# Kernel optimization log

Measured on AMD Instinct MI355X. Metric: run time of the kernel, lower is better.

Reference implementation:

```python
import jax, jax.numpy as jnp
import numpy as np

B, C, H, W = 16, 256, 56, 56
WH, WW = 7, 7
NH = 8            # heads
HID = 1024        # mlp hidden = int(4*dim)
N = WH * WW
EPS = 1e-5


def _rel_index():
    # mirrors the torch buffer computation in Rel_Attention.__init__
    coords = np.stack(np.meshgrid(np.arange(WH), np.arange(WW), indexing='ij')).reshape(2, -1)  # (2, N)
    rel = coords[:, :, None] - coords[:, None, :]  # (2, N, N)
    rel[0] += WH - 1
    rel[1] += WW - 1
    rel[0] *= 2 * WW - 1
    return jnp.asarray(rel.sum(0).reshape(-1))  # (N*N,)

REL_IDX = _rel_index()


def channel_ln(x, w, b):
    # LayerNorm over channel dim of NCHW tensor (permute -> LN -> permute back)
    xt = x.transpose(0, 2, 3, 1)  # BHWC
    mu = xt.mean(-1, keepdims=True)
    var = xt.var(-1, keepdims=True)
    xt = (xt - mu) / jnp.sqrt(var + EPS) * w + b
    return xt.transpose(0, 3, 1, 2)


def to_blocks(x):
    # (B,C,H,W) -> (B, H/wh, W/ww, C, wh, ww)
    b, c, h, w = x.shape
    x = x.reshape(b, c, h // WH, WH, w // WW, WW)
    return x.transpose(0, 2, 4, 1, 3, 5)


def unblock(x):
    # faithful to original: reshape(B, C, Hb*win_W, Hb*win_W)  (square sizes)
    b, hb, wb, c, wh, ww = x.shape
    return x.transpose(0, 3, 1, 4, 2, 5).reshape(b, c, hb * ww, hb * ww)


def rel_attention(xw, qkv_w, qkv_b, proj_w, proj_b, table):
    b, hb, wb, c = xw.shape[:4]
    hd = c // NH
    scale = hd ** (-0.5)
    xf = xw.reshape(-1, c, N)                                  # (M, C, N)
    qkv = jnp.einsum('oc,mcn->mon', qkv_w, xf) + qkv_b[None, :, None]
    q, k, v = jnp.split(qkv, 3, axis=1)

    def heads(t):
        return t.reshape(-1, NH, hd, N).transpose(0, 1, 3, 2)  # (M, h, N, d)

    q, k, v = heads(q), heads(k), heads(v)
    bias = table[REL_IDX].reshape(N, N, NH).transpose(2, 0, 1)  # (h, N, N)
    attn = jnp.einsum('mhnd,mhkd->mhnk', q, k) * scale + bias
    attn = jax.nn.softmax(attn, axis=-1)
    o = jnp.einsum('mhnk,mhkd->mhnd', attn, v)                 # (M, h, N, d)
    o = o.transpose(0, 1, 3, 2).reshape(-1, c, N)              # (M, C, N)
    o = jnp.einsum('oc,mcn->mon', proj_w, o) + proj_b[None, :, None]
    return o.reshape(b, hb, wb, c, WH, WW)


def mlp(x, fc1_w, fc1_b, fc2_w, fc2_b):
    h = jnp.einsum('oc,bchw->bohw', fc1_w, x) + fc1_b[None, :, None, None]
    h = jax.nn.gelu(h, approximate=False)
    return jnp.einsum('oc,bchw->bohw', fc2_w, h) + fc2_b[None, :, None, None]


def setup_inputs() -> dict:
    key = jax.random.key(0)
    ks = jax.random.split(key, 8)
    s = 0.02
    return {
        'x': jax.random.normal(ks[0], (B, C, H, W), jnp.float32),
        'ln1_w': jnp.ones((C,), jnp.float32),
        'ln1_b': jnp.zeros((C,), jnp.float32),
        'ln2_w': jnp.ones((C,), jnp.float32),
        'ln2_b': jnp.zeros((C,), jnp.float32),
        'qkv_w': jax.random.normal(ks[1], (3 * C, C), jnp.float32) * s,
        'qkv_b': jnp.zeros((3 * C,), jnp.float32),
        'proj_w': jax.random.normal(ks[2], (C, C), jnp.float32) * s,
        'proj_b': jnp.zeros((C,), jnp.float32),
        'rel_bias_table': jax.random.normal(ks[3], ((2 * WH - 1) * (2 * WW - 1), NH), jnp.float32) * s,
        'fc1_w': jax.random.normal(ks[4], (HID, C), jnp.float32) * s,
        'fc1_b': jnp.zeros((HID,), jnp.float32),
        'fc2_w': jax.random.normal(ks[5], (C, HID), jnp.float32) * s,
        'fc2_b': jnp.zeros((C,), jnp.float32),
    }


def reference(x, ln1_w, ln1_b, ln2_w, ln2_b, qkv_w, qkv_b, proj_w, proj_b,
              rel_bias_table, fc1_w, fc1_b, fc2_w, fc2_b):
    out = to_blocks(channel_ln(x, ln1_w, ln1_b))
    out = rel_attention(out, qkv_w, qkv_b, proj_w, proj_b, rel_bias_table)
    # original applies attn a second time before unblocking
    out = rel_attention(out, qkv_w, qkv_b, proj_w, proj_b, rel_bias_table)
    x = x + unblock(out)
    x = x + mlp(channel_ln(x, ln2_w, ln2_b), fc1_w, fc1_b, fc2_w, fc2_b)
    return x
```

## Files before the change

### kernel.cpp

```cpp
#include <hip/hip_runtime.h>
#include <stdint.h>

typedef uint16_t u16;
typedef short bf16x4 __attribute__((ext_vector_type(4)));
typedef short bf16x8 __attribute__((ext_vector_type(8)));
typedef float f32x4 __attribute__((ext_vector_type(4)));

__device__ __forceinline__ float bf2f(u16 s) {
  union { unsigned int i; float f; } c; c.i = ((unsigned int)s) << 16; return c.f;
}
__device__ __forceinline__ u16 f2bf(float f) {
  union { float f; unsigned int i; } c; c.f = f;
  unsigned int u = c.i;
  u += 0x7FFFu + ((u >> 16) & 1u);
  return (u16)(u >> 16);
}
__device__ __forceinline__ f32x4 mfma16(bf16x8 a, bf16x8 b, f32x4 c) {
  return __builtin_amdgcn_mfma_f32_16x16x32_bf16(a, b, c, 0, 0, 0);
}
__device__ __forceinline__ int dtype_flag(const u16* ln1w_raw) { return ln1w_raw[0] == 0x3F80 ? 1 : 0; }
__device__ __forceinline__ float loadF(const void* p, size_t i, int flag) {
  return flag ? bf2f(((const u16*)p)[i]) : ((const float*)p)[i];
}

#define OFF_QKVW 0
#define OFF_QKVB 196608
#define OFF_PROJW 197376
#define OFF_PROJB 262912
#define OFF_REL 263168
#define OFF_FC1W 264520
#define OFF_FC1B 526664
#define OFF_FC2W 527688
#define OFF_FC2B 789832
#define OFF_LN1W 790088
#define OFF_LN1B 790344
#define OFF_LN2W 790600
#define OFF_LN2B 790856
#define WC_TOTAL 791112

__global__ __launch_bounds__(256) void k_convert(const u16* __restrict__ ln1w_raw,
    const void* qkvw, const void* qkvb, const void* projw, const void* projb,
    const void* rel, const void* fc1w, const void* fc1b, const void* fc2w, const void* fc2b,
    const void* ln1w, const void* ln1b, const void* ln2w, const void* ln2b,
    u16* __restrict__ dst) {
  const int flag = dtype_flag(ln1w_raw);
  int i = blockIdx.x * 256 + threadIdx.x;
  if (i >= WC_TOTAL) return;
  const void* src; int off;
  if      (i < OFF_QKVB)  { src = qkvw;  off = i - OFF_QKVW; }
  else if (i < OFF_PROJW) { src = qkvb;  off = i - OFF_QKVB; }
  else if (i < OFF_PROJB) { src = projw; off = i - OFF_PROJW; }
  else if (i < OFF_REL)   { src = projb; off = i - OFF_PROJB; }
  else if (i < OFF_FC1W)  { src = rel;   off = i - OFF_REL; }
  else if (i < OFF_FC1B)  { src = fc1w;  off = i - OFF_FC1W; }
  else if (i < OFF_FC2W)  { src = fc1b;  off = i - OFF_FC1B; }
  else if (i < OFF_FC2B)  { src = fc2w;  off = i - OFF_FC2W; }
  else if (i < OFF_LN1W)  { src = fc2b;  off = i - OFF_FC2B; }
  else if (i < OFF_LN1B)  { src = ln1w;  off = i - OFF_LN1W; }
  else if (i < OFF_LN2W)  { src = ln1b;  off = i - OFF_LN1B; }
  else if (i < OFF_LN2B)  { src = ln2w;  off = i - OFF_LN2W; }
  else                    { src = ln2b;  off = i - OFF_LN2B; }
  if (i < OFF_QKVB) {
    int j = off & 7, li = (off >> 3) & 63, c0i = (off >> 9) & 7, grp = off >> 12;
    off = (grp * 16 + (li & 15)) * 256 + c0i * 32 + (li >> 4) * 8 + j;
  } else if (i >= OFF_PROJW && i < OFF_PROJB) {
    int j = off & 7, li = (off >> 3) & 63, c0i = (off >> 9) & 7, grp = off >> 12;
    off = (grp * 16 + (li & 15)) * 256 + c0i * 32 + (li >> 4) * 8 + j;
  } else if (i >= OFF_FC1W && i < OFF_FC1B) {
    int j = off & 7, li = (off >> 3) & 63, hj = (off >> 9) & 1, c0i = (off >> 10) & 7,
        w = (off >> 13) & 3, ch = off >> 15;
    off = (ch * 128 + w * 32 + hj * 16 + (li & 15)) * 256 + c0i * 32 + (li >> 4) * 8 + j;
  } else if (i >= OFF_FC2W && i < OFF_FC2B) {
    int j = off & 7, li = (off >> 3) & 63, oct = (off >> 9) & 3, kki = (off >> 11) & 3,
        ch = (off >> 13) & 7, w = off >> 16;
    off = (w * 64 + oct * 16 + (li & 15)) * 1024 + ch * 128 + kki * 32 + (li >> 4) * 8 + j;
  }
  dst[i] = flag ? ((const u16*)src)[off] : f2bf(((const float*)src)[off]);
}

__global__ __launch_bounds__(256) void k_ln1b(const void* __restrict__ xin,
                                              const u16* __restrict__ ln1w_raw,
                                              const u16* __restrict__ lw,
                                              const u16* __restrict__ lb,
                                              u16* __restrict__ win) {
  const int flag = dtype_flag(ln1w_raw);
  __shared__ float tile[56 * 257];
  __shared__ float smu[56], srs[56];
  const int bid = blockIdx.x;
  const int b = bid / 56, h = bid - b * 56;
  const int t = threadIdx.x;
  const int hb = h / 7, ph = h - hb * 7;
  if (!flag) {
#pragma unroll
    for (int i = 0; i < 14; ++i) {
      int chunk = i * 256 + t;
      int c = chunk / 14, w4 = (chunk - c * 14) * 4;
      const float* xp4 = (const float*)xin + ((size_t)(b * 256 + c) * 56 + h) * 56 + w4;
      f32x4 v = *(const f32x4*)xp4;
#pragma unroll
      for (int k = 0; k < 4; ++k) tile[(w4 + k) * 257 + c] = v[k];
    }
  } else {
#pragma unroll
    for (int i = 0; i < 7; ++i) {
      int chunk = i * 256 + t;
      int c = chunk / 7, w8 = (chunk - c * 7) * 8;
      const u16* xp8 = (const u16*)xin + ((size_t)(b * 256 + c) * 56 + h) * 56 + w8;
      bf16x8 v = *(const bf16x8*)xp8;
#pragma unroll
      for (int k = 0; k < 8; ++k) tile[(w8 + k) * 257 + c] = bf2f((u16)v[k]);
    }
  }
  __syncthreads();
  {
    const int row = t >> 2, qq = t & 3;
    float s = 0.f, q = 0.f;
    if (row < 56) {
      const float* tr = &tile[row * 257 + qq];
#pragma unroll 8
      for (int c0 = 0; c0 < 64; ++c0) { float v = tr[c0 * 4]; s += v; q += v * v; }
    }
    s += __shfl_xor(s, 1, 64); q += __shfl_xor(q, 1, 64);
    s += __shfl_xor(s, 2, 64); q += __shfl_xor(q, 2, 64);
    if (row < 56 && qq == 0) {
      float mm = s * (1.f / 256.f);
      float var = q * (1.f / 256.f) - mm * mm;
      smu[row] = mm; srs[row] = rsqrtf(var + 1e-5f);
    }
  }
  __syncthreads();
#pragma unroll
  for (int i = 0; i < 7; ++i) {
    int eid8 = i * 256 + t;
    int wp = eid8 >> 5, c8 = (eid8 & 31) << 3;
    const float mm = smu[wp], rs = srs[wp];
    const int m = b * 64 + hb * 8 + (wp / 7), n = ph * 7 + (wp % 7);
    bf16x8 o;
#pragma unroll
    for (int j = 0; j < 8; ++j) {
      int c = c8 + j;
      o[j] = (short)f2bf((tile[wp * 257 + c] - mm) * rs * bf2f(lw[c]) + bf2f(lb[c]));
    }
    *(bf16x8*)&win[(size_t)m * 12544 + n * 256 + c8] = o;
  }
}

__global__ __launch_bounds__(512) void k_attn_stage(const u16* __restrict__ win,
                                                    const u16* __restrict__ qkvw,
                                                    const u16* __restrict__ qkvb,
                                                    const u16* __restrict__ rel,
                                                    const u16* __restrict__ projw,
                                                    const u16* __restrict__ projb,
                                                    u16* __restrict__ wout) {
  __shared__ __align__(16) u16 xs[64 * 264];
  __shared__ __align__(16) u16 wa[8][7424];
  const int m = blockIdx.x;
  const int t = threadIdx.x;
  const int w = t >> 6, li = t & 63, lane = li & 15, quad = li >> 4;
  const int hg = w;
  const f32x4 z = {0.f, 0.f, 0.f, 0.f};
  const u16* src = win + (size_t)m * 12544;
#pragma unroll
  for (int i = 0; i < 4; ++i) {
    int chunk = i * 512 + t;
    if (chunk < 1568) {
      int n = chunk >> 5, cc = (chunk & 31) << 3;
      *(bf16x8*)&xs[n * 264 + cc] = *(const bf16x8*)&src[chunk << 3];
    }
  }
  for (int i = t; i < 15 * 264; i += 512) xs[49 * 264 + i] = 0;
  u16* qw = wa[w];
  u16* kw = wa[w] + 2560;
  u16* vw = wa[w] + 5120;
  u16* Pw = wa[w];
  u16* Os = xs;
  for (int i = li; i < 15 * 40; i += 64) { qw[49 * 40 + i] = 0; kw[49 * 40 + i] = 0; }
  for (int i = li; i < 32 * 15; i += 64) { int d = i / 15, j = i - d * 15; vw[d * 72 + 49 + j] = 0; }
  __syncthreads();
  const float SCALE = 0.17677669529663687f;
#pragma unroll
  for (int part = 0; part < 2; ++part) {
    const int obase = part * 256 + hg * 32;
    f32x4 acc[4][2];
#pragma unroll
    for (int i = 0; i < 4; ++i) { acc[i][0] = z; acc[i][1] = z; }
#pragma unroll
    for (int c0i = 0; c0i < 8; ++c0i) {
      bf16x8 a[4], b[2];
#pragma unroll
      for (int nt = 0; nt < 4; ++nt)
        a[nt] = *(const bf16x8*)&xs[(nt * 16 + lane) * 264 + c0i * 32 + quad * 8];
#pragma unroll
      for (int oj = 0; oj < 2; ++oj)
        b[oj] = *(const bf16x8*)&qkvw[(size_t)(((part * 16 + hg * 2 + oj) * 8 + c0i) * 64 + li) * 8];
      __builtin_amdgcn_s_setprio(1);
#pragma unroll
      for (int nt = 0; nt < 4; ++nt)
#pragma unroll
        for (int oj = 0; oj < 2; ++oj) acc[nt][oj] = mfma16(a[nt], b[oj], acc[nt][oj]);
      __builtin_amdgcn_s_setprio(0);
    }
    u16* dstL = part ? kw : qw;
#pragma unroll
    for (int oj = 0; oj < 2; ++oj) {
      const int d = oj * 16 + lane;
      const float bias = bf2f(qkvb[obase + d]);
#pragma unroll
      for (int nt = 0; nt < 4; ++nt)
#pragma unroll
        for (int r = 0; r < 4; ++r) {
          int n = nt * 16 + quad * 4 + r;
          if (n < 49) dstL[n * 40 + d] = f2bf(acc[nt][oj][r] + bias);
        }
    }
  }
  {
    f32x4 acc[2][4];
#pragma unroll
    for (int i = 0; i < 2; ++i)
#pragma unroll
      for (int j = 0; j < 4; ++j) acc[i][j] = z;
#pragma unroll
    for (int c0i = 0; c0i < 8; ++c0i) {
      bf16x8 a[2], b[4];
#pragma unroll
      for (int vj = 0; vj < 2; ++vj)
        a[vj] = *(const bf16x8*)&qkvw[(size_t)(((32 + hg * 2 + vj) * 8 + c0i) * 64 + li) * 8];
#pragma unroll
      for (int nt = 0; nt < 4; ++nt)
        b[nt] = *(const bf16x8*)&xs[(nt * 16 + lane) * 264 + c0i * 32 + quad * 8];
      __builtin_amdgcn_s_setprio(1);
#pragma unroll
      for (int vj = 0; vj < 2; ++vj)
#pragma unroll
        for (int nt = 0; nt < 4; ++nt) acc[vj][nt] = mfma16(a[vj], b[nt], acc[vj][nt]);
      __builtin_amdgcn_s_setprio(0);
    }
#pragma unroll
    for (int vj = 0; vj < 2; ++vj)
#pragma unroll
      for (int r = 0; r < 4; ++r) {
        const int d = vj * 16 + quad * 4 + r;
        const float bias = bf2f(qkvb[512 + hg * 32 + d]);
#pragma unroll
        for (int nt = 0; nt < 4; ++nt) {
          int n = nt * 16 + lane;
          if (n < 49) vw[d * 72 + n] = f2bf(acc[vj][nt][r] + bias);
        }
      }
  }
  __syncthreads();
  f32x4 s[4][4];
  {
    bf16x8 aq[4], bk[4];
#pragma unroll
    for (int nt = 0; nt < 4; ++nt) {
      aq[nt] = *(const bf16x8*)&qw[(nt * 16 + lane) * 40 + quad * 8];
      bk[nt] = *(const bf16x8*)&kw[(nt * 16 + lane) * 40 + quad * 8];
    }
    __builtin_amdgcn_s_setprio(1);
#pragma unroll
    for (int i = 0; i < 4; ++i)
#pragma unroll
      for (int j = 0; j < 4; ++j) s[i][j] = mfma16(aq[i], bk[j], z);
    __builtin_amdgcn_s_setprio(0);
  }
#pragma unroll
  for (int nt1 = 0; nt1 < 4; ++nt1) {
#pragma unroll
    for (int r = 0; r < 4; ++r) {
      int n1 = nt1 * 16 + quad * 4 + r;
      int n1c = n1 < 49 ? n1 : 48;
      int ph1 = n1c / 7, pw1 = n1c - ph1 * 7;
#pragma unroll
      for (int j = 0; j < 4; ++j) {
        int n2 = j * 16 + lane;
        float e;
        if (n2 < 49) {
          int ph2 = n2 / 7, pw2 = n2 - ph2 * 7;
          int idx = (ph1 - ph2 + 6) * 13 + (pw1 - pw2 + 6);
          e = __expf(s[nt1][j][r] * SCALE + bf2f(rel[idx * 8 + hg]));
        } else e = 0.f;
        Pw[n1 * 72 + j * 16 + lane] = f2bf(e);
      }
    }
  }
  {
    f32x4 o[4][2], ssum[4];
#pragma unroll
    for (int i = 0; i < 4; ++i) { o[i][0] = z; o[i][1] = z; ssum[i] = z; }
    bf16x8 bones;
#pragma unroll
    for (int k = 0; k < 8; ++k) bones[k] = (short)0x3F80;
#pragma unroll
    for (int kc = 0; kc < 2; ++kc) {
      bf16x8 ap[4], bv[2];
#pragma unroll
      for (int nt1 = 0; nt1 < 4; ++nt1)
        ap[nt1] = *(const bf16x8*)&Pw[(nt1 * 16 + lane) * 72 + kc * 32 + quad * 8];
#pragma unroll
      for (int dt = 0; dt < 2; ++dt)
        bv[dt] = *(const bf16x8*)&vw[(dt * 16 + lane) * 72 + kc * 32 + quad * 8];
      __builtin_amdgcn_s_setprio(1);
#pragma unroll
      for (int nt1 = 0; nt1 < 4; ++nt1) {
        ssum[nt1] = mfma16(ap[nt1], bones, ssum[nt1]);
#pragma unroll
        for (int dt = 0; dt < 2; ++dt) o[nt1][dt] = mfma16(ap[nt1], bv[dt], o[nt1][dt]);
      }
      __builtin_amdgcn_s_setprio(0);
    }
#pragma unroll
    for (int nt1 = 0; nt1 < 4; ++nt1) {
      f32x4 rv;
#pragma unroll
      for (int r = 0; r < 4; ++r) rv[r] = __builtin_amdgcn_rcpf(ssum[nt1][r]);
#pragma unroll
      for (int dt = 0; dt < 2; ++dt)
#pragma unroll
        for (int r = 0; r < 4; ++r) {
          int n1 = nt1 * 16 + quad * 4 + r;
          if (n1 < 49) Os[n1 * 264 + hg * 32 + dt * 16 + lane] = f2bf(o[nt1][dt][r] * rv[r]);
        }
    }
  }
  __syncthreads();
  {
    f32x4 acc[4][2];
#pragma unroll
    for (int i = 0; i < 4; ++i) { acc[i][0] = z; acc[i][1] = z; }
#pragma unroll
    for (int c0i = 0; c0i < 8; ++c0i) {
      bf16x8 a[4], b[2];
#pragma unroll
      for (int nt = 0; nt < 4; ++nt)
        a[nt] = *(const bf16x8*)&Os[(nt * 16 + lane) * 264 + c0i * 32 + quad * 8];
#pragma unroll
      for (int oj = 0; oj < 2; ++oj)
        b[oj] = *(const bf16x8*)&projw[(size_t)(((w * 2 + oj) * 8 + c0i) * 64 + li) * 8];
      __builtin_amdgcn_s_setprio(1);
#pragma unroll
      for (int nt = 0; nt < 4; ++nt)
#pragma unroll
        for (int oj = 0; oj < 2; ++oj) acc[nt][oj] = mfma16(a[nt], b[oj], acc[nt][oj]);
      __builtin_amdgcn_s_setprio(0);
    }
#pragma unroll
    for (int oj = 0; oj < 2; ++oj) {
      const int oc = w * 32 + oj * 16 + lane;
      const float bias = bf2f(projb[oc]);
#pragma unroll
      for (int nt = 0; nt < 4; ++nt)
#pragma unroll
        for (int r = 0; r < 4; ++r) {
          int n = nt * 16 + quad * 4 + r;
          if (n < 49) wout[(size_t)m * 12544 + n * 256 + oc] = f2bf(acc[nt][oj][r] + bias);
        }
    }
  }
}

__global__ __launch_bounds__(256) void k_resid2(const void* __restrict__ xin,
                                                const u16* __restrict__ ln1w_raw,
                                                const u16* __restrict__ attn,
                                                const u16* __restrict__ l2w,
                                                const u16* __restrict__ l2b,
                                                u16* __restrict__ xrn,
                                                u16* __restrict__ ln2d) {
  const int flag = dtype_flag(ln1w_raw);
  __shared__ float tile[56 * 257];
  __shared__ float smu[56], srs[56];
  const int bid = blockIdx.x;
  const int b = bid / 56, h = bid - b * 56;
  const int t = threadIdx.x;
  const int hb = h / 7, ph = h - hb * 7;
#pragma unroll
  for (int i = 0; i < 7; ++i) {
    int eid8 = i * 256 + t;
    int wp = eid8 >> 5, c8 = (eid8 & 31) << 3;
    int mm = b * 64 + hb * 8 + (wp / 7), nn = ph * 7 + (wp % 7);
    bf16x8 v = *(const bf16x8*)&attn[(size_t)mm * 12544 + nn * 256 + c8];
    float* dst = &tile[wp * 257 + c8];
#pragma unroll
    for (int j = 0; j < 8; ++j) dst[j] = bf2f((u16)v[j]);
  }
  __syncthreads();
  if (!flag) {
#pragma unroll
    for (int i = 0; i < 14; ++i) {
      int chunk = i * 256 + t;
      int c = chunk / 14, w4 = (chunk - c * 14) * 4;
      const size_t base = ((size_t)(b * 256 + c) * 56 + h) * 56 + w4;
      f32x4 xv = *(const f32x4*)((const float*)xin + base);
      bf16x4 o4;
#pragma unroll
      for (int k = 0; k < 4; ++k) {
        float v = tile[(w4 + k) * 257 + c] + xv[k];
        tile[(w4 + k) * 257 + c] = v;
        o4[k] = (short)f2bf(v);
      }
      *(bf16x4*)&xrn[base] = o4;
    }
  } else {
#pragma unroll
    for (int i = 0; i < 7; ++i) {
      int chunk = i * 256 + t;
      int c = chunk / 7, w8 = (chunk - c * 7) * 8;
      const size_t base = ((size_t)(b * 256 + c) * 56 + h) * 56 + w8;
      bf16x8 xv = *(const bf16x8*)((const u16*)xin + base);
      bf16x8 o8;
#pragma unroll
      for (int k = 0; k < 8; ++k) {
        float v = tile[(w8 + k) * 257 + c] + bf2f((u16)xv[k]);
        tile[(w8 + k) * 257 + c] = v;
        o8[k] = (short)f2bf(v);
      }
      *(bf16x8*)&xrn[base] = o8;
    }
  }
  __syncthreads();
  {
    const int row = t >> 2, qq = t & 3;
    float s = 0.f, q = 0.f;
    if (row < 56) {
      const float* tr = &tile[row * 257 + qq];
#pragma unroll 8
      for (int c0 = 0; c0 < 64; ++c0) { float v = tr[c0 * 4]; s += v; q += v * v; }
    }
    s += __shfl_xor(s, 1, 64); q += __shfl_xor(q, 1, 64);
    s += __shfl_xor(s, 2, 64); q += __shfl_xor(q, 2, 64);
    if (row < 56 && qq == 0) {
      float mm = s * (1.f / 256.f);
      float var = q * (1.f / 256.f) - mm * mm;
      smu[row] = mm; srs[row] = rsqrtf(var + 1e-5f);
    }
  }
  __syncthreads();
#pragma unroll
  for (int i = 0; i < 7; ++i) {
    int eid8 = i * 256 + t;
    int wp = eid8 >> 5, c8 = (eid8 & 31) << 3;
    const float mm = smu[wp], rs = srs[wp];
    bf16x8 o;
#pragma unroll
    for (int j = 0; j < 8; ++j) {
      int c = c8 + j;
      o[j] = (short)f2bf((tile[wp * 257 + c] - mm) * rs * bf2f(l2w[c]) + bf2f(l2b[c]));
    }
    const int p = b * 3136 + h * 56 + wp;
    const int pblk = p >> 6, pt = (p & 63) >> 4, r16 = p & 15;
    const int c0i = c8 >> 5, quad = (c8 >> 3) & 3;
    *(bf16x8*)&ln2d[(size_t)((((pblk * 4 + pt) * 8 + c0i) * 64 + quad * 16 + r16)) << 3] = o;
  }
}

__global__ __launch_bounds__(256, 3) void k_mlp2(const u16* __restrict__ aG,
                                                 const u16* __restrict__ w1,
                                                 const u16* __restrict__ b1,
                                                 const u16* __restrict__ w2,
                                                 const u16* __restrict__ b2,
                                                 const u16* __restrict__ xrn,
                                                 const u16* __restrict__ ln1w_raw,
                                                 void* __restrict__ out) {
  const int flag = dtype_flag(ln1w_raw);
  __shared__ __align__(16) u16 arena[25088];
  u16* xp = arena;
  u16* g  = arena + 16384;
  const int pblk = blockIdx.x;
  const int pix0 = pblk * 64;
  const int t = threadIdx.x;
  const int w = t >> 6, li = t & 63, lane = li & 15, quad = li >> 4;
  {
    const u16* asrc = aG + (size_t)pblk * 16384;
#pragma unroll
    for (int i = 0; i < 8; ++i) {
      int idx = i * 256 + t;
      *(bf16x8*)&xp[idx * 8] = *(const bf16x8*)&asrc[(size_t)idx * 8];
    }
  }
  __syncthreads();
  const f32x4 z = {0.f, 0.f, 0.f, 0.f};
  f32x4 acc2[4][4];
#pragma unroll
  for (int i = 0; i < 4; ++i)
#pragma unroll
    for (int j = 0; j < 4; ++j) acc2[i][j] = z;

  auto fc1 = [&](int ch) {
    f32x4 a1[4][2];
#pragma unroll
    for (int i = 0; i < 4; ++i) { a1[i][0] = z; a1[i][1] = z; }
#pragma unroll
    for (int c0i = 0; c0i < 8; ++c0i) {
      bf16x8 av[4], bw[2];
#pragma unroll
      for (int pt = 0; pt < 4; ++pt)
        av[pt] = *(const bf16x8*)&xp[((pt * 8 + c0i) * 64 + li) * 8];
#pragma unroll
      for (int hj = 0; hj < 2; ++hj)
        bw[hj] = *(const bf16x8*)&w1[(size_t)((((ch * 4 + w) * 8 + c0i) * 2 + hj) * 64 + li) * 8];
#pragma unroll
      for (int pt = 0; pt < 4; ++pt)
#pragma unroll
        for (int hj = 0; hj < 2; ++hj) a1[pt][hj] = mfma16(av[pt], bw[hj], a1[pt][hj]);
    }
#pragma unroll
    for (int hj = 0; hj < 2; ++hj) {
      const int hl = w * 32 + hj * 16 + lane;
      const float bias = bf2f(b1[ch * 128 + hl]);
#pragma unroll
      for (int pt = 0; pt < 4; ++pt)
#pragma unroll
        for (int r = 0; r < 4; ++r) {
          float u_ = a1[pt][hj][r] + bias;
          float y = u_ * fmaf(u_ * u_, 0.035677408136300125f, 0.7978845608028654f);
          float e2 = __expf(-2.f * y);
          float v = u_ * __builtin_amdgcn_rcpf(1.f + e2);
          g[(pt * 16 + quad * 4 + r) * 136 + hl] = f2bf(v);
        }
    }
  };
  auto fc2 = [&](int ch) {
#pragma unroll
    for (int kki = 0; kki < 4; ++kki) {
      bf16x8 aw[4], bg[4];
#pragma unroll
      for (int oct = 0; oct < 4; ++oct)
        aw[oct] = *(const bf16x8*)&w2[(size_t)((((w * 8 + ch) * 4 + kki) * 4 + oct) * 64 + li) * 8];
#pragma unroll
      for (int pt = 0; pt < 4; ++pt)
        bg[pt] = *(const bf16x8*)&g[(pt * 16 + lane) * 136 + kki * 32 + quad * 8];
#pragma unroll
      for (int oct = 0; oct < 4; ++oct)
#pragma unroll
        for (int pt = 0; pt < 4; ++pt) acc2[oct][pt] = mfma16(aw[oct], bg[pt], acc2[oct][pt]);
    }
  };

  fc1(0);
  __syncthreads();
#pragma unroll 1
  for (int ch = 0; ch < 8; ++ch) {
    fc2(ch);
    if (ch < 7) {
      __syncthreads();
      fc1(ch + 1);
      __syncthreads();
    }
  }

  float* Ob = (float*)arena;
  const int b_ = pix0 / 3136, rem0 = pix0 - b_ * 3136;
  const int sub = t & 7, r0 = t >> 3;
#pragma unroll 1
  for (int e = 0; e < 2; ++e) {
    __syncthreads();
    if ((w >> 1) == e) {
      const int wl = w & 1;
#pragma unroll
      for (int oct = 0; oct < 4; ++oct)
#pragma unroll
        for (int pt = 0; pt < 4; ++pt)
#pragma unroll
          for (int r = 0; r < 4; ++r)
            Ob[(wl * 64 + oct * 16 + quad * 4 + r) * 65 + pt * 16 + lane] = acc2[oct][pt][r];
    }
    __syncthreads();
    bf16x8 xr[4];
    size_t addrs[4];
#pragma unroll
    for (int i = 0; i < 4; ++i) {
      const int oc = e * 128 + i * 32 + r0;
      addrs[i] = (size_t)(b_ * 256 + oc) * 3136 + rem0 + sub * 8;
      xr[i] = *(const bf16x8*)&xrn[addrs[i]];
    }
#pragma unroll
    for (int i = 0; i < 4; ++i) {
      const int oc = e * 128 + i * 32 + r0;
      const float bias = bf2f(b2[oc]);
      const float* obr = &Ob[(i * 32 + r0) * 65 + sub * 8];
      float v[8];
#pragma unroll
      for (int j = 0; j < 8; ++j)
        v[j] = obr[j] + bias + bf2f((u16)xr[i][j]);
      if (flag) {
        bf16x8 o8;
#pragma unroll
        for (int j = 0; j < 8; ++j) o8[j] = (short)f2bf(v[j]);
        *(bf16x8*)&((u16*)out)[addrs[i]] = o8;
      } else {
        float* dst = &((float*)out)[addrs[i]];
        f32x4 lo = {v[0], v[1], v[2], v[3]}, hi = {v[4], v[5], v[6], v[7]};
        *(f32x4*)&dst[0] = lo;
        *(f32x4*)&dst[4] = hi;
      }
    }
  }
}

extern "C" void kernel_launch(void* const* d_in, const int* in_sizes, int n_in,
                              void* d_out, int out_size, void* d_ws, size_t ws_size,
                              hipStream_t stream) {
  (void)in_sizes; (void)n_in; (void)out_size; (void)ws_size;
  const void* x     = d_in[0];
  const u16* ln1w_raw = (const u16*)d_in[1];
  u16* ws = (u16*)d_ws;
  const size_t R = 12845056;
  u16* R0 = ws;
  u16* R1 = ws + R;
  u16* R2 = ws + 2 * R;
  u16* WC = ws + 3 * R;
  const u16* qkvw_c = WC + OFF_QKVW;
  const u16* qkvb_c = WC + OFF_QKVB;
  const u16* projw_c = WC + OFF_PROJW;
  const u16* projb_c = WC + OFF_PROJB;
  const u16* rel_c  = WC + OFF_REL;
  const u16* fc1w_c = WC + OFF_FC1W;
  const u16* fc1b_c = WC + OFF_FC1B;
  const u16* fc2w_c = WC + OFF_FC2W;
  const u16* fc2b_c = WC + OFF_FC2B;
  const u16* ln1w_c = WC + OFF_LN1W;
  const u16* ln1b_c = WC + OFF_LN1B;
  const u16* ln2w_c = WC + OFF_LN2W;
  const u16* ln2b_c = WC + OFF_LN2B;

  k_convert<<<(WC_TOTAL + 255) / 256, 256, 0, stream>>>(
      ln1w_raw, d_in[5], d_in[6], d_in[7], d_in[8], d_in[9],
      d_in[10], d_in[11], d_in[12], d_in[13], d_in[1], d_in[2], d_in[3], d_in[4], WC);

  k_ln1b      <<<896, 256, 0, stream>>>(x, ln1w_raw, ln1w_c, ln1b_c, R0);
  k_attn_stage<<<1024, 512, 0, stream>>>(R0, qkvw_c, qkvb_c, rel_c, projw_c, projb_c, R1);
  k_attn_stage<<<1024, 512, 0, stream>>>(R1, qkvw_c, qkvb_c, rel_c, projw_c, projb_c, R2);
  k_resid2    <<<896, 256, 0, stream>>>(x, ln1w_raw, R2, ln2w_c, ln2b_c, R0, R1);
  k_mlp2      <<<784, 256, 0, stream>>>(R1, fc1w_c, fc1b_c, fc2w_c, fc2b_c, R0, ln1w_raw, d_out);
}
```

Baseline: 424.0 us.

## Split attention stage into per-head-half core and separate projection kernels with fragment layout

The fused 512-thread attention kernel is split into a 256-thread attention core (two blocks per window, four heads each) and a separate projection kernel. Intermediate window activations are stored in an MFMA-fragment-ordered layout so the core can read its A/B fragments directly from global memory, without staging them in LDS or synchronising the whole block. The goal is lower LDS use and higher occupancy for the attention part. The cost is extra kernel launches, a global round-trip for the attention output, and each window's input being read twice, once per block.

```diff
diff --git a/kernel.cpp b/kernel.cpp
--- a/kernel.cpp
+++ b/kernel.cpp
@@ -21,6 +21,11 @@
 __device__ __forceinline__ int dtype_flag(const u16* ln1w_raw) { return ln1w_raw[0] == 0x3F80 ? 1 : 0; }
 __device__ __forceinline__ float loadF(const void* p, size_t i, int flag) {
   return flag ? bf2f(((const u16*)p)[i]) : ((const float*)p)[i];
+}
+
+__device__ __forceinline__ int frag_idx8(int n, int c0, int qc) {
+  return (n < 48) ? (((n >> 4) * 8 + c0) * 64 + (n & 15) + 16 * qc)
+                  : (1536 + c0 * 4 + qc);
 }
 
 #define OFF_QKVW 0
@@ -141,43 +146,34 @@
       int c = c8 + j;
       o[j] = (short)f2bf((tile[wp * 257 + c] - mm) * rs * bf2f(lw[c]) + bf2f(lb[c]));
     }
-    *(bf16x8*)&win[(size_t)m * 12544 + n * 256 + c8] = o;
-  }
-}
-
-__global__ __launch_bounds__(512) void k_attn_stage(const u16* __restrict__ win,
-                                                    const u16* __restrict__ qkvw,
-                                                    const u16* __restrict__ qkvb,
-                                                    const u16* __restrict__ rel,
-                                                    const u16* __restrict__ projw,
-                                                    const u16* __restrict__ projb,
-                                                    u16* __restrict__ wout) {
-  __shared__ __align__(16) u16 xs[64 * 264];
-  __shared__ __align__(16) u16 wa[8][7424];
-  const int m = blockIdx.x;
+    const int idx8 = frag_idx8(n, c8 >> 5, (c8 >> 3) & 3);
+    *(bf16x8*)&win[(size_t)m * 12544 + idx8 * 8] = o;
+  }
+}
+
+__global__ __launch_bounds__(256) void k_attn_core(const u16* __restrict__ win,
+                                                   const u16* __restrict__ qkvw,
+                                                   const u16* __restrict__ qkvb,
+                                                   const u16* __restrict__ rel,
+                                                   u16* __restrict__ Ofrag) {
+  __shared__ __align__(16) u16 wa[4][7424];
+  const int blk = blockIdx.x;
+  const int m = blk >> 1;
   const int t = threadIdx.x;
   const int w = t >> 6, li = t & 63, lane = li & 15, quad = li >> 4;
-  const int hg = w;
+  const int hg = (blk & 1) * 4 + w;
   const f32x4 z = {0.f, 0.f, 0.f, 0.f};
-  const u16* src = win + (size_t)m * 12544;
-#pragma unroll
-  for (int i = 0; i < 4; ++i) {
-    int chunk = i * 512 + t;
-    if (chunk < 1568) {
-      int n = chunk >> 5, cc = (chunk & 31) << 3;
-      *(bf16x8*)&xs[n * 264 + cc] = *(const bf16x8*)&src[chunk << 3];
-    }
-  }
-  for (int i = t; i < 15 * 264; i += 512) xs[49 * 264 + i] = 0;
+  const u16* winm = win + (size_t)m * 12544;
   u16* qw = wa[w];
   u16* kw = wa[w] + 2560;
   u16* vw = wa[w] + 5120;
   u16* Pw = wa[w];
-  u16* Os = xs;
-  for (int i = li; i < 15 * 40; i += 64) { qw[49 * 40 + i] = 0; kw[49 * 40 + i] = 0; }
-  for (int i = li; i < 32 * 15; i += 64) { int d = i / 15, j = i - d * 15; vw[d * 72 + 49 + j] = 0; }
-  __syncthreads();
+  for (int i = li; i < 32 * 15; i += 64) { int d = i / 15, jn = i - d * 15; vw[d * 72 + 49 + jn] = 0; }
   const float SCALE = 0.17677669529663687f;
+  auto xfrag = [&](int nt, int c0i) -> bf16x8 {
+    int idx8 = (nt < 3) ? ((nt * 8 + c0i) * 64 + li) : (1536 + c0i * 4 + quad);
+    return *(const bf16x8*)&winm[(size_t)idx8 * 8];
+  };
 #pragma unroll
   for (int part = 0; part < 2; ++part) {
     const int obase = part * 256 + hg * 32;
@@ -188,8 +184,7 @@
     for (int c0i = 0; c0i < 8; ++c0i) {
       bf16x8 a[4], b[2];
 #pragma unroll
-      for (int nt = 0; nt < 4; ++nt)
-        a[nt] = *(const bf16x8*)&xs[(nt * 16 + lane) * 264 + c0i * 32 + quad * 8];
+      for (int nt = 0; nt < 4; ++nt) a[nt] = xfrag(nt, c0i);
 #pragma unroll
       for (int oj = 0; oj < 2; ++oj)
         b[oj] = *(const bf16x8*)&qkvw[(size_t)(((part * 16 + hg * 2 + oj) * 8 + c0i) * 64 + li) * 8];
@@ -227,8 +222,7 @@
       for (int vj = 0; vj < 2; ++vj)
         a[vj] = *(const bf16x8*)&qkvw[(size_t)(((32 + hg * 2 + vj) * 8 + c0i) * 64 + li) * 8];
 #pragma unroll
-      for (int nt = 0; nt < 4; ++nt)
-        b[nt] = *(const bf16x8*)&xs[(nt * 16 + lane) * 264 + c0i * 32 + quad * 8];
+      for (int nt = 0; nt < 4; ++nt) b[nt] = xfrag(nt, c0i);
       __builtin_amdgcn_s_setprio(1);
 #pragma unroll
       for (int vj = 0; vj < 2; ++vj)
@@ -249,7 +243,6 @@
         }
       }
   }
-  __syncthreads();
   f32x4 s[4][4];
   {
     bf16x8 aq[4], bk[4];
@@ -320,43 +313,75 @@
 #pragma unroll
         for (int r = 0; r < 4; ++r) {
           int n1 = nt1 * 16 + quad * 4 + r;
-          if (n1 < 49) Os[n1 * 264 + hg * 32 + dt * 16 + lane] = f2bf(o[nt1][dt][r] * rv[r]);
+          if (n1 < 49) {
+            int c_ = hg * 32 + dt * 16 + lane;
+            int idx8 = frag_idx8(n1, hg, (c_ >> 3) & 3);
+            Ofrag[(size_t)m * 12544 + idx8 * 8 + (c_ & 7)] = f2bf(o[nt1][dt][r] * rv[r]);
+          }
         }
     }
   }
-  __syncthreads();
-  {
-    f32x4 acc[4][2];
-#pragma unroll
-    for (int i = 0; i < 4; ++i) { acc[i][0] = z; acc[i][1] = z; }
-#pragma unroll
-    for (int c0i = 0; c0i < 8; ++c0i) {
-      bf16x8 a[4], b[2];
-#pragma unroll
-      for (int nt = 0; nt < 4; ++nt)
-        a[nt] = *(const bf16x8*)&Os[(nt * 16 + lane) * 264 + c0i * 32 + quad * 8];
-#pragma unroll
-      for (int oj = 0; oj < 2; ++oj)
-        b[oj] = *(const bf16x8*)&projw[(size_t)(((w * 2 + oj) * 8 + c0i) * 64 + li) * 8];
-      __builtin_amdgcn_s_setprio(1);
-#pragma unroll
-      for (int nt = 0; nt < 4; ++nt)
-#pragma unroll
-        for (int oj = 0; oj < 2; ++oj) acc[nt][oj] = mfma16(a[nt], b[oj], acc[nt][oj]);
-      __builtin_amdgcn_s_setprio(0);
-    }
-#pragma unroll
-    for (int oj = 0; oj < 2; ++oj) {
-      const int oc = w * 32 + oj * 16 + lane;
-      const float bias = bf2f(projb[oc]);
-#pragma unroll
-      for (int nt = 0; nt < 4; ++nt)
-#pragma unroll
-        for (int r = 0; r < 4; ++r) {
-          int n = nt * 16 + quad * 4 + r;
-          if (n < 49) wout[(size_t)m * 12544 + n * 256 + oc] = f2bf(acc[nt][oj][r] + bias);
+}
+
+__global__ __launch_bounds__(256) void k_proj(const u16* __restrict__ Ofrag,
+                                              const u16* __restrict__ projw,
+                                              const u16* __restrict__ projb,
+                                              u16* __restrict__ out,
+                                              int out_frag) {
+  __shared__ __align__(16) u16 os[12544];
+  const int m = blockIdx.x;
+  const int t = threadIdx.x;
+  const int w = t >> 6, li = t & 63, lane = li & 15, quad = li >> 4;
+  const u16* src = Ofrag + (size_t)m * 12544;
+#pragma unroll
+  for (int i = 0; i < 7; ++i) {
+    int chunk = i * 256 + t;
+    if (chunk < 1568) *(bf16x8*)&os[chunk * 8] = *(const bf16x8*)&src[(size_t)chunk * 8];
+  }
+  __syncthreads();
+  const f32x4 z = {0.f, 0.f, 0.f, 0.f};
+  f32x4 acc[4][4];
+#pragma unroll
+  for (int i = 0; i < 4; ++i)
+#pragma unroll
+    for (int j = 0; j < 4; ++j) acc[i][j] = z;
+#pragma unroll
+  for (int c0i = 0; c0i < 8; ++c0i) {
+    bf16x8 a[4], b[4];
+#pragma unroll
+    for (int nt = 0; nt < 4; ++nt) {
+      int idx8 = (nt < 3) ? ((nt * 8 + c0i) * 64 + li) : (1536 + c0i * 4 + quad);
+      a[nt] = *(const bf16x8*)&os[idx8 * 8];
+    }
+#pragma unroll
+    for (int oj = 0; oj < 4; ++oj)
+      b[oj] = *(const bf16x8*)&projw[(size_t)(((w * 4 + oj) * 8 + c0i) * 64 + li) * 8];
+    __builtin_amdgcn_s_setprio(1);
+#pragma unroll
+    for (int nt = 0; nt < 4; ++nt)
+#pragma unroll
+      for (int oj = 0; oj < 4; ++oj) acc[nt][oj] = mfma16(a[nt], b[oj], acc[nt][oj]);
+    __builtin_amdgcn_s_setprio(0);
+  }
+#pragma unroll
+  for (int oj = 0; oj < 4; ++oj) {
+    const int oc = (w * 4 + oj) * 16 + lane;
+    const float bias = bf2f(projb[oc]);
+#pragma unroll
+    for (int nt = 0; nt < 4; ++nt)
+#pragma unroll
+      for (int r = 0; r < 4; ++r) {
+        int n = nt * 16 + quad * 4 + r;
+        if (n < 49) {
+          u16 val = f2bf(acc[nt][oj][r] + bias);
+          if (!out_frag) {
+            out[(size_t)m * 12544 + n * 256 + oc] = val;
+          } else {
+            int idx8 = frag_idx8(n, oc >> 5, (oc >> 3) & 3);
+            out[(size_t)m * 12544 + idx8 * 8 + (oc & 7)] = val;
+          }
         }
-    }
+      }
   }
 }
 
@@ -628,9 +653,11 @@
       ln1w_raw, d_in[5], d_in[6], d_in[7], d_in[8], d_in[9],
       d_in[10], d_in[11], d_in[12], d_in[13], d_in[1], d_in[2], d_in[3], d_in[4], WC);
 
-  k_ln1b      <<<896, 256, 0, stream>>>(x, ln1w_raw, ln1w_c, ln1b_c, R0);
-  k_attn_stage<<<1024, 512, 0, stream>>>(R0, qkvw_c, qkvb_c, rel_c, projw_c, projb_c, R1);
-  k_attn_stage<<<1024, 512, 0, stream>>>(R1, qkvw_c, qkvb_c, rel_c, projw_c, projb_c, R2);
-  k_resid2    <<<896, 256, 0, stream>>>(x, ln1w_raw, R2, ln2w_c, ln2b_c, R0, R1);
-  k_mlp2      <<<784, 256, 0, stream>>>(R1, fc1w_c, fc1b_c, fc2w_c, fc2b_c, R0, ln1w_raw, d_out);
-}
+  k_ln1b     <<<896, 256, 0, stream>>>(x, ln1w_raw, ln1w_c, ln1b_c, R0);
+  k_attn_core<<<2048, 256, 0, stream>>>(R0, qkvw_c, qkvb_c, rel_c, R1);
+  k_proj     <<<1024, 256, 0, stream>>>(R1, projw_c, projb_c, R2, 1);
+  k_attn_core<<<2048, 256, 0, stream>>>(R2, qkvw_c, qkvb_c, rel_c, R1);
+  k_proj     <<<1024, 256, 0, stream>>>(R1, projw_c, projb_c, R0, 0);
+  k_resid2   <<<896, 256, 0, stream>>>(x, ln1w_raw, R0, ln2w_c, ln2b_c, R2, R1);
+  k_mlp2     <<<784, 256, 0, stream>>>(R1, fc1w_c, fc1b_c, fc2w_c, fc2b_c, R2, ln1w_raw, d_out);
+}
```

Result: slower. 476.6 us (+12.4%).

## Store window activations in MFMA fragment order and keep attention output per-wave

Applied to the files above, without the earlier changes.

LN1 and the first attention stage now write window activations in an MFMA-fragment-major layout. The attention kernel can then load them with a linear copy and read operands without padded row strides or zero fill. Each wave keeps its attention output in its own LDS scratch region rather than the shared xs buffer, which drops one block-wide barrier and shrinks the xs allocation. The extra output-index arithmetic and the row-48 replication for padding rows add some cost and complexity.

```diff
diff --git a/kernel.cpp b/kernel.cpp
--- a/kernel.cpp
+++ b/kernel.cpp
@@ -21,6 +21,11 @@
 __device__ __forceinline__ int dtype_flag(const u16* ln1w_raw) { return ln1w_raw[0] == 0x3F80 ? 1 : 0; }
 __device__ __forceinline__ float loadF(const void* p, size_t i, int flag) {
   return flag ? bf2f(((const u16*)p)[i]) : ((const float*)p)[i];
+}
+
+__device__ __forceinline__ int frag_idx8(int n, int c0, int qc) {
+  return (n < 48) ? (((n >> 4) * 8 + c0) * 64 + (n & 15) + 16 * qc)
+                  : (1536 + c0 * 4 + qc);
 }
 
 #define OFF_QKVW 0
@@ -141,7 +146,8 @@
       int c = c8 + j;
       o[j] = (short)f2bf((tile[wp * 257 + c] - mm) * rs * bf2f(lw[c]) + bf2f(lb[c]));
     }
-    *(bf16x8*)&win[(size_t)m * 12544 + n * 256 + c8] = o;
+    const int idx8 = frag_idx8(n, c8 >> 5, (c8 >> 3) & 3);
+    *(bf16x8*)&win[(size_t)m * 12544 + idx8 * 8] = o;
   }
 }
 
@@ -151,8 +157,9 @@
                                                     const u16* __restrict__ rel,
                                                     const u16* __restrict__ projw,
                                                     const u16* __restrict__ projb,
-                                                    u16* __restrict__ wout) {
-  __shared__ __align__(16) u16 xs[64 * 264];
+                                                    u16* __restrict__ wout,
+                                                    int out_frag) {
+  __shared__ __align__(16) u16 xs[12544];
   __shared__ __align__(16) u16 wa[8][7424];
   const int m = blockIdx.x;
   const int t = threadIdx.x;
@@ -163,21 +170,21 @@
 #pragma unroll
   for (int i = 0; i < 4; ++i) {
     int chunk = i * 512 + t;
-    if (chunk < 1568) {
-      int n = chunk >> 5, cc = (chunk & 31) << 3;
-      *(bf16x8*)&xs[n * 264 + cc] = *(const bf16x8*)&src[chunk << 3];
-    }
-  }
-  for (int i = t; i < 15 * 264; i += 512) xs[49 * 264 + i] = 0;
+    if (chunk < 1568) *(bf16x8*)&xs[chunk * 8] = *(const bf16x8*)&src[(size_t)chunk * 8];
+  }
   u16* qw = wa[w];
   u16* kw = wa[w] + 2560;
   u16* vw = wa[w] + 5120;
   u16* Pw = wa[w];
-  u16* Os = xs;
+  u16* Ow = wa[w];
   for (int i = li; i < 15 * 40; i += 64) { qw[49 * 40 + i] = 0; kw[49 * 40 + i] = 0; }
-  for (int i = li; i < 32 * 15; i += 64) { int d = i / 15, j = i - d * 15; vw[d * 72 + 49 + j] = 0; }
+  for (int i = li; i < 32 * 15; i += 64) { int d = i / 15, jn = i - d * 15; vw[d * 72 + 49 + jn] = 0; }
   __syncthreads();
   const float SCALE = 0.17677669529663687f;
+  auto xfrag = [&](int nt, int c0i) -> bf16x8 {
+    int idx8 = (nt < 3) ? ((nt * 8 + c0i) * 64 + li) : (1536 + c0i * 4 + quad);
+    return *(const bf16x8*)&xs[idx8 * 8];
+  };
 #pragma unroll
   for (int part = 0; part < 2; ++part) {
     const int obase = part * 256 + hg * 32;
@@ -188,8 +195,7 @@
     for (int c0i = 0; c0i < 8; ++c0i) {
       bf16x8 a[4], b[2];
 #pragma unroll
-      for (int nt = 0; nt < 4; ++nt)
-        a[nt] = *(const bf16x8*)&xs[(nt * 16 + lane) * 264 + c0i * 32 + quad * 8];
+      for (int nt = 0; nt < 4; ++nt) a[nt] = xfrag(nt, c0i);
 #pragma unroll
       for (int oj = 0; oj < 2; ++oj)
         b[oj] = *(const bf16x8*)&qkvw[(size_t)(((part * 16 + hg * 2 + oj) * 8 + c0i) * 64 + li) * 8];
@@ -227,8 +233,7 @@
       for (int vj = 0; vj < 2; ++vj)
         a[vj] = *(const bf16x8*)&qkvw[(size_t)(((32 + hg * 2 + vj) * 8 + c0i) * 64 + li) * 8];
 #pragma unroll
-      for (int nt = 0; nt < 4; ++nt)
-        b[nt] = *(const bf16x8*)&xs[(nt * 16 + lane) * 264 + c0i * 32 + quad * 8];
+      for (int nt = 0; nt < 4; ++nt) b[nt] = xfrag(nt, c0i);
       __builtin_amdgcn_s_setprio(1);
 #pragma unroll
       for (int vj = 0; vj < 2; ++vj)
@@ -249,7 +254,6 @@
         }
       }
   }
-  __syncthreads();
   f32x4 s[4][4];
   {
     bf16x8 aq[4], bk[4];
@@ -320,7 +324,7 @@
 #pragma unroll
         for (int r = 0; r < 4; ++r) {
           int n1 = nt1 * 16 + quad * 4 + r;
-          if (n1 < 49) Os[n1 * 264 + hg * 32 + dt * 16 + lane] = f2bf(o[nt1][dt][r] * rv[r]);
+          if (n1 < 49) Ow[n1 * 40 + dt * 16 + lane] = f2bf(o[nt1][dt][r] * rv[r]);
         }
     }
   }
@@ -334,7 +338,7 @@
       bf16x8 a[4], b[2];
 #pragma unroll
       for (int nt = 0; nt < 4; ++nt)
-        a[nt] = *(const bf16x8*)&Os[(nt * 16 + lane) * 264 + c0i * 32 + quad * 8];
+        a[nt] = *(const bf16x8*)&wa[c0i][(nt * 16 + lane) * 40 + quad * 8];
 #pragma unroll
       for (int oj = 0; oj < 2; ++oj)
         b[oj] = *(const bf16x8*)&projw[(size_t)(((w * 2 + oj) * 8 + c0i) * 64 + li) * 8];
@@ -354,7 +358,15 @@
 #pragma unroll
         for (int r = 0; r < 4; ++r) {
           int n = nt * 16 + quad * 4 + r;
-          if (n < 49) wout[(size_t)m * 12544 + n * 256 + oc] = f2bf(acc[nt][oj][r] + bias);
+          if (n < 49) {
+            u16 val = f2bf(acc[nt][oj][r] + bias);
+            if (!out_frag) {
+              wout[(size_t)m * 12544 + n * 256 + oc] = val;
+            } else {
+              int idx8 = frag_idx8(n, oc >> 5, (oc >> 3) & 3);
+              wout[(size_t)m * 12544 + idx8 * 8 + (oc & 7)] = val;
+            }
+          }
         }
     }
   }
@@ -629,8 +641,8 @@
       d_in[10], d_in[11], d_in[12], d_in[13], d_in[1], d_in[2], d_in[3], d_in[4], WC);
 
   k_ln1b      <<<896, 256, 0, stream>>>(x, ln1w_raw, ln1w_c, ln1b_c, R0);
-  k_attn_stage<<<1024, 512, 0, stream>>>(R0, qkvw_c, qkvb_c, rel_c, projw_c, projb_c, R1);
-  k_attn_stage<<<1024, 512, 0, stream>>>(R1, qkvw_c, qkvb_c, rel_c, projw_c, projb_c, R2);
+  k_attn_stage<<<1024, 512, 0, stream>>>(R0, qkvw_c, qkvb_c, rel_c, projw_c, projb_c, R1, 1);
+  k_attn_stage<<<1024, 512, 0, stream>>>(R1, qkvw_c, qkvb_c, rel_c, projw_c, projb_c, R2, 0);
   k_resid2    <<<896, 256, 0, stream>>>(x, ln1w_raw, R2, ln2w_c, ln2b_c, R0, R1);
   k_mlp2      <<<784, 256, 0, stream>>>(R1, fc1w_c, fc1b_c, fc2w_c, fc2b_c, R0, ln1w_raw, d_out);
 }
```

Result: no change. 426.6 us (+0.6%).
